# Kernel optimization log

Measured on AMD Instinct MI355X. Metric: run time of the kernel, lower is better.

Reference implementation:

```python
import jax, jax.numpy as jnp
import numpy as np

B, T = 64, 1024
S, O = 512, 32000


def setup_inputs() -> dict:
    key = jax.random.key(0)
    k1, k2, k3, k4 = jax.random.split(key, 4)
    return {
        "observations": jax.random.randint(k1, (B, T), 0, O),
        "state_transitions": jax.random.normal(k2, (S, S), dtype=jnp.float32),
        "observation_transitions": jax.random.normal(k3, (S, O), dtype=jnp.float32),
        "prior_states": jax.random.normal(k4, (S,), dtype=jnp.float32),
    }


def reference(observations, state_transitions, observation_transitions, prior_states):
    # Precompute log-softmaxed parameters once (torch code recomputed per step).
    log_trans = jax.nn.log_softmax(state_transitions, axis=-1)        # [S, S]
    log_obs = jax.nn.log_softmax(observation_transitions, axis=-1)    # [S, O]
    log_prior = jax.nn.log_softmax(prior_states)                      # [S]

    b = observations.shape[0]
    # torch code appends a terminal observation 0 at the end of each sequence
    obs_seq = jnp.concatenate(
        [observations, jnp.zeros((b, 1), dtype=observations.dtype)], axis=1
    )  # [B, T+1]

    # alpha_0[b, s] = log_obs[s, o_0(b)] + log_prior[s]
    alpha0 = log_obs[:, obs_seq[:, 0]].T + log_prior  # [B, S]

    def step(alpha, obs_t):
        # alpha[b, i] -> pred[b, j] = logsumexp_i(alpha[b, i] + log_trans[i, j])
        pred = jax.nn.logsumexp(alpha[:, :, None] + log_trans[None, :, :], axis=1)  # [B, S]
        new_alpha = log_obs[:, obs_t].T + pred  # [B, S]
        return new_alpha, None

    alpha, _ = jax.lax.scan(step, alpha0, obs_seq[:, 1:].T)  # scan over T steps
    return jax.nn.logsumexp(alpha, axis=1)  # [B]
```

## Files before the change

### kernel.cpp

```cpp
#include <hip/hip_runtime.h>
#include <hip/hip_bf16.h>
#include <cstdint>

#define SS 512
#define OBS_N 32000
#define TT 1024
#define BB 64

#define RPW 24
#define TPW 8

typedef _Float16 h2 __attribute__((ext_vector_type(2)));

static __device__ __forceinline__ float wave_max(float v) {
#pragma unroll
  for (int m = 32; m >= 1; m >>= 1) v = fmaxf(v, __shfl_xor(v, m, 64));
  return v;
}
static __device__ __forceinline__ float wave_sum(float v) {
#pragma unroll
  for (int m = 32; m >= 1; m >>= 1) v += __shfl_xor(v, m, 64);
  return v;
}

static __device__ __forceinline__ float wave_max_dpp(float x) {
  int v = __builtin_bit_cast(int, x);
#define DPP_STEP(ctrl)                                                        \
  {                                                                           \
    int t = __builtin_amdgcn_update_dpp(v, v, (ctrl), 0xf, 0xf, false);       \
    v = __builtin_bit_cast(                                                   \
        int, fmaxf(__builtin_bit_cast(float, v), __builtin_bit_cast(float, t)));\
  }
  DPP_STEP(0x111)
  DPP_STEP(0x112)
  DPP_STEP(0x114)
  DPP_STEP(0x118)
  DPP_STEP(0x142)
  DPP_STEP(0x143)
#undef DPP_STEP
  return __builtin_bit_cast(float, __builtin_amdgcn_readlane(v, 63));
}

static __device__ __forceinline__ float dot2f(h2 a, h2 b, float c) {
#if __has_builtin(__builtin_amdgcn_fdot2)
  return __builtin_amdgcn_fdot2(a, b, c, false);
#else
  return c + (float)a.x * (float)b.x + (float)a.y * (float)b.y;
#endif
}

static __device__ __forceinline__ h2 as_h2(uint32_t u) {
  return __builtin_bit_cast(h2, u);
}
static __device__ __forceinline__ uint32_t sel4(const uint4& v, int s) {
  return s == 0 ? v.x : s == 1 ? v.y : s == 2 ? v.z : v.w;
}

__global__ __launch_bounds__(256) void prep_obs_lse(const float* __restrict__ ot,
                                                    float* __restrict__ lse) {
  const int s = blockIdx.x;
  const int tid = threadIdx.x;
  const float4* row = (const float4*)(ot + (size_t)s * OBS_N);
  __shared__ float redm[4];
  __shared__ float reds[4];

  float m = -INFINITY;
  for (int k = tid; k < OBS_N / 4; k += 256) {
    float4 v = row[k];
    m = fmaxf(m, fmaxf(fmaxf(v.x, v.y), fmaxf(v.z, v.w)));
  }
  m = wave_max(m);
  if ((tid & 63) == 0) redm[tid >> 6] = m;
  __syncthreads();
  m = fmaxf(fmaxf(redm[0], redm[1]), fmaxf(redm[2], redm[3]));

  float ssum = 0.f;
  for (int k = tid; k < OBS_N / 4; k += 256) {
    float4 v = row[k];
    ssum += __expf(v.x - m) + __expf(v.y - m) + __expf(v.z - m) + __expf(v.w - m);
  }
  ssum = wave_sum(ssum);
  if ((tid & 63) == 0) reds[tid >> 6] = ssum;
  __syncthreads();
  if (tid == 0) {
    float s4 = reds[0] + reds[1] + reds[2] + reds[3];
    lse[s] = m + __logf(s4);
  }
}

__global__ __launch_bounds__(256) void transpose_ot(const float* __restrict__ ot,
                                                    float* __restrict__ oT) {
  __shared__ float tile[32][33];
  const int o0 = blockIdx.x * 32;
  const int j0 = blockIdx.y * 32;
  const int tx = threadIdx.x & 31;
  const int ty = threadIdx.x >> 5;
#pragma unroll
  for (int r = 0; r < 32; r += 8)
    tile[ty + r][tx] = ot[(size_t)(j0 + ty + r) * OBS_N + (o0 + tx)];
  __syncthreads();
#pragma unroll
  for (int r = 0; r < 32; r += 8)
    oT[(size_t)(o0 + ty + r) * SS + (j0 + tx)] = tile[tx][ty + r];
}

__global__ __launch_bounds__(512) void prep_trans(const float* __restrict__ st,
                                                  uint32_t* __restrict__ EP) {
  const int r = blockIdx.x;
  const int j = threadIdx.x;
  const int wv = j >> 6;
  float a0 = st[(size_t)(2 * r) * SS + j];
  float a1 = st[(size_t)(2 * r + 1) * SS + j];

  __shared__ float w0[8], w1[8], s0a[8], s1a[8];
  float m0 = wave_max(a0), m1 = wave_max(a1);
  if ((j & 63) == 0) { w0[wv] = m0; w1[wv] = m1; }
  __syncthreads();
  m0 = w0[0]; m1 = w1[0];
#pragma unroll
  for (int q = 1; q < 8; ++q) { m0 = fmaxf(m0, w0[q]); m1 = fmaxf(m1, w1[q]); }

  float e0 = __expf(a0 - m0), e1 = __expf(a1 - m1);
  float s0 = wave_sum(e0), s1 = wave_sum(e1);
  if ((j & 63) == 0) { s0a[wv] = s0; s1a[wv] = s1; }
  __syncthreads();
  s0 = 0.f; s1 = 0.f;
#pragma unroll
  for (int q = 0; q < 8; ++q) { s0 += s0a[q]; s1 += s1a[q]; }

  _Float16 h0 = (_Float16)(e0 / s0);
  _Float16 h1 = (_Float16)(e1 / s1);
  uint32_t u = ((uint32_t)__builtin_bit_cast(unsigned short, h1) << 16) |
               (uint32_t)__builtin_bit_cast(unsigned short, h0);
  EP[(size_t)r * SS + j] = u;
}

__global__ __launch_bounds__(512) void prep_prior(const float* __restrict__ pr,
                                                  float* __restrict__ lp) {
  const int j = threadIdx.x;
  const int wv = j >> 6;
  float a = pr[j];
  __shared__ float wm[8], ws[8];
  float m = wave_max(a);
  if ((j & 63) == 0) wm[wv] = m;
  __syncthreads();
  m = wm[0];
#pragma unroll
  for (int q = 1; q < 8; ++q) m = fmaxf(m, wm[q]);
  float e = __expf(a - m);
  float s = wave_sum(e);
  if ((j & 63) == 0) ws[wv] = s;
  __syncthreads();
  s = 0.f;
#pragma unroll
  for (int q = 0; q < 8; ++q) s += ws[q];
  lp[j] = a - m - __logf(s);
}

__attribute__((amdgpu_waves_per_eu(2, 2))) __global__ void
__launch_bounds__(512) hmm_main(
    const uint32_t* __restrict__ EP, const float* __restrict__ lse_obs,
    const float* __restrict__ lp, const int* __restrict__ obs,
    const float* __restrict__ og, int sO, int sJ, float* __restrict__ out) {
  __shared__ uint32_t eL[64][2][64][4];
  __shared__ __align__(16) unsigned short ph16[SS];
  __shared__ __align__(16) unsigned short ppb[2][8][SS];
  __shared__ __align__(16) float wred[2][8];
  __shared__ float fin_m[8], fin_s[8];

  const int tid = threadIdx.x;
  const int w = tid >> 6;
  const int l = tid & 63;
  const int b = blockIdx.x;
  const int j = tid;

  uint32_t eR[RPW * 8];
#pragma unroll
  for (int p = 0; p < RPW; ++p)
#pragma unroll
    for (int k = 0; k < 8; ++k)
      eR[p * 8 + k] = EP[(size_t)(32 * w + p) * SS + k * 64 + l];

  for (int idx = tid; idx < 64 * 2 * 64; idx += 512) {
    int tq = idx >> 7;
    int c = (idx >> 6) & 1;
    int ll = idx & 63;
    int pr = 32 * (tq >> 3) + RPW + (tq & 7);
    const uint32_t* src = EP + (size_t)pr * SS + c * 256 + ll;
    eL[tq][c][ll][0] = src[0];
    eL[tq][c][ll][1] = src[64];
    eL[tq][c][ll][2] = src[128];
    eL[tq][c][ll][3] = src[192];
  }

  const float lse_j = lse_obs[j];
  const float lpj = lp[j];
  const size_t jOff = (size_t)j * sJ;
  const int* orow = obs + b * TT;

  const int o0 = orow[0];
  float alpha = og[(size_t)o0 * sO + jOff] - lse_j + lpj;

  int on = orow[1];
  float otv = og[(size_t)on * sO + jOff];

  __syncthreads();

  for (int t = 1; t <= TT; ++t) {
    const int par = t & 1;

    int o2 = (t <= TT - 2) ? orow[t + 1] : 0;
    float ot_pf = (t < TT) ? og[(size_t)o2 * sO + jOff] : 0.f;

    float mw = wave_max_dpp(alpha);
    if (l == 0) wred[par][w] = mw;

    float Pj = __expf(alpha - mw);
    ph16[j] = __builtin_bit_cast(unsigned short, (_Float16)Pj);
    __builtin_amdgcn_wave_barrier();

    float acc[8] = {0.f, 0.f, 0.f, 0.f, 0.f, 0.f, 0.f, 0.f};

#pragma unroll
    for (int qg = 0; qg < 2; ++qg) {
      uint4 ph4 = *(const uint4*)&ph16[64 * w + 48 + 8 * qg];
#pragma unroll
      for (int s = 0; s < 4; ++s) {
        const int q = 4 * qg + s;
        h2 phv = as_h2(sel4(ph4, s));
        const uint4 c0 = *(const uint4*)&eL[w * 8 + q][0][l][0];
        const uint4 c1 = *(const uint4*)&eL[w * 8 + q][1][l][0];
        acc[0] = dot2f(phv, as_h2(c0.x), acc[0]);
        acc[1] = dot2f(phv, as_h2(c0.y), acc[1]);
        acc[2] = dot2f(phv, as_h2(c0.z), acc[2]);
        acc[3] = dot2f(phv, as_h2(c0.w), acc[3]);
        acc[4] = dot2f(phv, as_h2(c1.x), acc[4]);
        acc[5] = dot2f(phv, as_h2(c1.y), acc[5]);
        acc[6] = dot2f(phv, as_h2(c1.z), acc[6]);
        acc[7] = dot2f(phv, as_h2(c1.w), acc[7]);
      }
    }

#pragma unroll
    for (int g = 0; g < 6; ++g) {
      uint4 ph4 = *(const uint4*)&ph16[64 * w + 8 * g];
#pragma unroll
      for (int s = 0; s < 4; ++s) {
        const int p = 4 * g + s;
        h2 phv = as_h2(sel4(ph4, s));
#pragma unroll
        for (int k = 0; k < 8; ++k)
          acc[k] = dot2f(phv, as_h2(eR[p * 8 + k]), acc[k]);
      }
    }

#pragma unroll
    for (int k = 0; k < 8; ++k)
      ppb[par][w][k * 64 + l] =
          __builtin_bit_cast(unsigned short, (_Float16)acc[k]);

    __syncthreads();

    const float4 wv0 = *(const float4*)&wred[par][0];
    const float4 wv1 = *(const float4*)&wred[par][4];
    float M = fmaxf(fmaxf(fmaxf(wv0.x, wv0.y), fmaxf(wv0.z, wv0.w)),
                    fmaxf(fmaxf(wv1.x, wv1.y), fmaxf(wv1.z, wv1.w)));
    float earg = wred[par][l & 7];
    float ee = __expf(earg - M);

    float pred = 0.f;
#pragma unroll
    for (int q = 0; q < 8; ++q) {
      float eq = __builtin_bit_cast(
          float, __builtin_amdgcn_readlane(__builtin_bit_cast(int, ee), q));
      float pq = (float)__builtin_bit_cast(_Float16, ppb[par][q][j]);
      pred = fmaf(eq, pq, pred);
    }
    alpha = M + __logf(pred) + (otv - lse_j);
    otv = ot_pf;
  }

  float m = wave_max(alpha);
  if (l == 0) fin_m[w] = m;
  __syncthreads();
  float M = fin_m[0];
#pragma unroll
  for (int q = 1; q < 8; ++q) M = fmaxf(M, fin_m[q]);
  float e = __expf(alpha - M);
  float s = wave_sum(e);
  if (l == 0) fin_s[w] = s;
  __syncthreads();
  if (tid == 0) {
    float tot = 0.f;
#pragma unroll
    for (int q = 0; q < 8; ++q) tot += fin_s[q];
    out[b] = M + __logf(tot);
  }
}

extern "C" void kernel_launch(void* const* d_in, const int* in_sizes, int n_in,
                              void* d_out, int out_size, void* d_ws, size_t ws_size,
                              hipStream_t stream) {
  const int* obs = (const int*)d_in[0];
  const float* st = (const float*)d_in[1];
  const float* ot = (const float*)d_in[2];
  const float* pr = (const float*)d_in[3];
  float* out = (float*)d_out;

  char* ws = (char*)d_ws;
  uint32_t* EP = (uint32_t*)ws;
  float* lse_obs = (float*)(ws + 524288);
  float* lprior = (float*)(ws + 526336);
  float* oT = (float*)(ws + 528384);
  const size_t need = 528384 + (size_t)OBS_N * SS * sizeof(float);

  prep_obs_lse<<<SS, 256, 0, stream>>>(ot, lse_obs);
  prep_trans<<<SS / 2, SS, 0, stream>>>(st, EP);
  prep_prior<<<1, SS, 0, stream>>>(pr, lprior);

  const float* og = ot;
  int sO = 1, sJ = OBS_N;
  if (ws_size >= need) {
    transpose_ot<<<dim3(OBS_N / 32, SS / 32), 256, 0, stream>>>(ot, oT);
    og = oT; sO = SS; sJ = 1;
  }
  hmm_main<<<BB, SS, 0, stream>>>(EP, lse_obs, lprior, obs, og, sO, sJ, out);
}
```

Before: 1.861 ms.

## Split per-step matvec across 16 waves with half-column ownership per wave

Moves the block from 512 to 1024 threads, giving each pair of waves one 64-state input slice, with each wave of the pair covering half of the 512 output columns. This halves per-thread register storage of transition weights and the dot-product work per step, aiming to shorten the serial per-step latency. In exchange, the final pred/alpha stage is now computed redundantly by both waves of each pair, and more threads take part in every block-wide barrier.

Result: slower. 2.034 ms (+9.3%).

```diff
diff --git a/kernel.cpp b/kernel.cpp
--- a/kernel.cpp
+++ b/kernel.cpp
@@ -7,8 +7,9 @@
 #define TT 1024
 #define BB 64
 
-#define RPW 24
-#define TPW 8
+#define RPP 24
+#define LPP 8
+#define NW 16
 
 typedef _Float16 h2 __attribute__((ext_vector_type(2)));
 
@@ -157,13 +158,12 @@
   lp[j] = a - m - __logf(s);
 }
 
-__attribute__((amdgpu_waves_per_eu(2, 2))) __global__ void
-__launch_bounds__(512) hmm_main(
+__global__ __launch_bounds__(1024, 4) void hmm_main(
     const uint32_t* __restrict__ EP, const float* __restrict__ lse_obs,
     const float* __restrict__ lp, const int* __restrict__ obs,
     const float* __restrict__ og, int sO, int sJ, float* __restrict__ out) {
-  __shared__ uint32_t eL[64][2][64][4];
-  __shared__ __align__(16) unsigned short ph16[SS];
+  __shared__ __align__(16) uint32_t eL[8][LPP][2][64][4];
+  __shared__ __align__(16) unsigned short ph16[NW][64];
   __shared__ __align__(16) unsigned short ppb[2][8][SS];
   __shared__ __align__(16) float wred[2][8];
   __shared__ float fin_m[8], fin_s[8];
@@ -171,38 +171,36 @@
   const int tid = threadIdx.x;
   const int w = tid >> 6;
   const int l = tid & 63;
-  const int b = blockIdx.x;
-  const int j = tid;
-
-  uint32_t eR[RPW * 8];
-#pragma unroll
-  for (int p = 0; p < RPW; ++p)
-#pragma unroll
-    for (int k = 0; k < 8; ++k)
-      eR[p * 8 + k] = EP[(size_t)(32 * w + p) * SS + k * 64 + l];
-
-  for (int idx = tid; idx < 64 * 2 * 64; idx += 512) {
-    int tq = idx >> 7;
-    int c = (idx >> 6) & 1;
-    int ll = idx & 63;
-    int pr = 32 * (tq >> 3) + RPW + (tq & 7);
-    const uint32_t* src = EP + (size_t)pr * SS + c * 256 + ll;
-    eL[tq][c][ll][0] = src[0];
-    eL[tq][c][ll][1] = src[64];
-    eL[tq][c][ll][2] = src[128];
-    eL[tq][c][ll][3] = src[192];
-  }
-
-  const float lse_j = lse_obs[j];
-  const float lpj = lp[j];
-  const size_t jOff = (size_t)j * sJ;
-  const int* orow = obs + b * TT;
-
-  const int o0 = orow[0];
-  float alpha = og[(size_t)o0 * sO + jOff] - lse_j + lpj;
-
-  int on = orow[1];
-  float otv = og[(size_t)on * sO + jOff];
+  const int b = w & 7;
+  const int h = w >> 3;
+  const int bb = blockIdx.x;
+  const int cP = 64 * b + l;
+
+  uint32_t eR[RPP * 4];
+#pragma unroll
+  for (int p = 0; p < RPP; ++p)
+#pragma unroll
+    for (int k = 0; k < 4; ++k)
+      eR[p * 4 + k] = EP[(size_t)(32 * b + p) * SS + 256 * h + 64 * k + l];
+
+#pragma unroll
+  for (int q = 0; q < LPP; ++q) {
+    const uint32_t* src = EP + (size_t)(32 * b + RPP + q) * SS + 256 * h + l;
+    uint4 v;
+    v.x = src[0];
+    v.y = src[64];
+    v.z = src[128];
+    v.w = src[192];
+    *(uint4*)&eL[b][q][h][l][0] = v;
+  }
+
+  const float lse_j = lse_obs[cP];
+  const float lpj = lp[cP];
+  const size_t jOff = (size_t)cP * sJ;
+  const int* orow = obs + bb * TT;
+
+  float alpha = og[(size_t)orow[0] * sO + jOff] - lse_j + lpj;
+  float otv = og[(size_t)orow[1] * sO + jOff];
 
   __syncthreads();
 
@@ -213,50 +211,46 @@
     float ot_pf = (t < TT) ? og[(size_t)o2 * sO + jOff] : 0.f;
 
     float mw = wave_max_dpp(alpha);
-    if (l == 0) wred[par][w] = mw;
+    if (l == 0 && h == 0) wred[par][b] = mw;
 
     float Pj = __expf(alpha - mw);
-    ph16[j] = __builtin_bit_cast(unsigned short, (_Float16)Pj);
+    ph16[w][l] = __builtin_bit_cast(unsigned short, (_Float16)Pj);
     __builtin_amdgcn_wave_barrier();
 
-    float acc[8] = {0.f, 0.f, 0.f, 0.f, 0.f, 0.f, 0.f, 0.f};
+    float acc[4] = {0.f, 0.f, 0.f, 0.f};
+    const uint32_t* phu = (const uint32_t*)&ph16[w][0];
 
 #pragma unroll
     for (int qg = 0; qg < 2; ++qg) {
-      uint4 ph4 = *(const uint4*)&ph16[64 * w + 48 + 8 * qg];
+      uint4 ph4 = *(const uint4*)&phu[RPP + 4 * qg];
 #pragma unroll
       for (int s = 0; s < 4; ++s) {
         const int q = 4 * qg + s;
         h2 phv = as_h2(sel4(ph4, s));
-        const uint4 c0 = *(const uint4*)&eL[w * 8 + q][0][l][0];
-        const uint4 c1 = *(const uint4*)&eL[w * 8 + q][1][l][0];
-        acc[0] = dot2f(phv, as_h2(c0.x), acc[0]);
-        acc[1] = dot2f(phv, as_h2(c0.y), acc[1]);
-        acc[2] = dot2f(phv, as_h2(c0.z), acc[2]);
-        acc[3] = dot2f(phv, as_h2(c0.w), acc[3]);
-        acc[4] = dot2f(phv, as_h2(c1.x), acc[4]);
-        acc[5] = dot2f(phv, as_h2(c1.y), acc[5]);
-        acc[6] = dot2f(phv, as_h2(c1.z), acc[6]);
-        acc[7] = dot2f(phv, as_h2(c1.w), acc[7]);
+        const uint4 ev = *(const uint4*)&eL[b][q][h][l][0];
+        acc[0] = dot2f(phv, as_h2(ev.x), acc[0]);
+        acc[1] = dot2f(phv, as_h2(ev.y), acc[1]);
+        acc[2] = dot2f(phv, as_h2(ev.z), acc[2]);
+        acc[3] = dot2f(phv, as_h2(ev.w), acc[3]);
       }
     }
 
 #pragma unroll
     for (int g = 0; g < 6; ++g) {
-      uint4 ph4 = *(const uint4*)&ph16[64 * w + 8 * g];
+      uint4 ph4 = *(const uint4*)&phu[4 * g];
 #pragma unroll
       for (int s = 0; s < 4; ++s) {
         const int p = 4 * g + s;
         h2 phv = as_h2(sel4(ph4, s));
 #pragma unroll
-        for (int k = 0; k < 8; ++k)
-          acc[k] = dot2f(phv, as_h2(eR[p * 8 + k]), acc[k]);
+        for (int k = 0; k < 4; ++k)
+          acc[k] = dot2f(phv, as_h2(eR[p * 4 + k]), acc[k]);
       }
     }
 
 #pragma unroll
-    for (int k = 0; k < 8; ++k)
-      ppb[par][w][k * 64 + l] =
+    for (int k = 0; k < 4; ++k)
+      ppb[par][b][256 * h + 64 * k + l] =
           __builtin_bit_cast(unsigned short, (_Float16)acc[k]);
 
     __syncthreads();
@@ -273,7 +267,7 @@
     for (int q = 0; q < 8; ++q) {
       float eq = __builtin_bit_cast(
           float, __builtin_amdgcn_readlane(__builtin_bit_cast(int, ee), q));
-      float pq = (float)__builtin_bit_cast(_Float16, ppb[par][q][j]);
+      float pq = (float)__builtin_bit_cast(_Float16, ppb[par][q][cP]);
       pred = fmaf(eq, pq, pred);
     }
     alpha = M + __logf(pred) + (otv - lse_j);
@@ -281,20 +275,20 @@
   }
 
   float m = wave_max(alpha);
-  if (l == 0) fin_m[w] = m;
+  if (l == 0 && h == 0) fin_m[b] = m;
   __syncthreads();
   float M = fin_m[0];
 #pragma unroll
   for (int q = 1; q < 8; ++q) M = fmaxf(M, fin_m[q]);
   float e = __expf(alpha - M);
   float s = wave_sum(e);
-  if (l == 0) fin_s[w] = s;
+  if (l == 0 && h == 0) fin_s[b] = s;
   __syncthreads();
   if (tid == 0) {
     float tot = 0.f;
 #pragma unroll
     for (int q = 0; q < 8; ++q) tot += fin_s[q];
-    out[b] = M + __logf(tot);
+    out[bb] = M + __logf(tot);
   }
 }
 
@@ -324,5 +318,5 @@
     transpose_ot<<<dim3(OBS_N / 32, SS / 32), 256, 0, stream>>>(ot, oT);
     og = oT; sO = SS; sJ = 1;
   }
-  hmm_main<<<BB, SS, 0, stream>>>(EP, lse_obs, lprior, obs, og, sO, sJ, out);
-}
+  hmm_main<<<BB, 1024, 0, stream>>>(EP, lse_obs, lprior, obs, og, sO, sJ, out);
+}
```
